# Kernel tuning notes

Measured on AMD Instinct MI355X. Metric: run time of the kernel, lower is better.

Reference implementation:

```python
import jax, jax.numpy as jnp
import numpy as np

B = 64          # graphs in batch
NVARS = 256     # variables per graph
LITS_PER = 2 * NVARS
NL = B * LITS_PER      # 32768 literals
CLS_PER = 1024
NC = B * CLS_PER       # 65536 clauses
K = 3                  # literals per clause (3-CNF)
D = 128
NUM_ITERS = 8


def setup_inputs() -> dict:
    key = jax.random.key(0)
    ks = jax.random.split(key, 16)
    # edge list of the sparse clause-literal incidence matrix adj_t [NC, NL]
    edge_clause = jnp.repeat(jnp.arange(NC, dtype=jnp.int32), K)            # [E]
    clause_graph = jnp.repeat(jnp.arange(NC, dtype=jnp.int32) // CLS_PER, K)
    lit_local = jax.random.randint(ks[0], (NC * K,), 0, LITS_PER, dtype=jnp.int32)
    edge_lit = clause_graph * LITS_PER + lit_local                          # [E]
    s = 0.05
    inp = {
        "edge_clause": edge_clause,
        "edge_lit": edge_lit,
        "x_l0": jax.random.uniform(ks[1], (NL, D), jnp.float32),
        "x_c0": jax.random.uniform(ks[2], (NC, D), jnp.float32),
        "W_ih_lc": jax.random.normal(ks[3], (D, D), jnp.float32) * s,
        "W_hh_lc": jax.random.normal(ks[4], (D, D), jnp.float32) * s,
        "b_ih_lc": jax.random.normal(ks[5], (D,), jnp.float32) * s,
        "b_hh_lc": jax.random.normal(ks[6], (D,), jnp.float32) * s,
        "W_ih_cl": jax.random.normal(ks[7], (D, 2 * D), jnp.float32) * s,
        "W_hh_cl": jax.random.normal(ks[8], (D, D), jnp.float32) * s,
        "b_ih_cl": jax.random.normal(ks[9], (D,), jnp.float32) * s,
        "b_hh_cl": jax.random.normal(ks[10], (D,), jnp.float32) * s,
        "L_vote_w": jax.random.normal(ks[11], (1, D), jnp.float32) * s,
        "L_vote_b": jax.random.normal(ks[12], (1,), jnp.float32) * s,
        "true_vec_w": jax.random.normal(ks[13], (1, D), jnp.float32) * s,
        "num_iters": NUM_ITERS,
    }
    return inp


def _l2norm(x):
    return x / jnp.linalg.norm(x, axis=1, keepdims=True)


def _rnn_cell(x, h, Wih, Whh, bih, bhh):
    # torch nn.RNN (tanh) single step: h' = tanh(x W_ih^T + b_ih + h W_hh^T + b_hh)
    return jnp.tanh(x @ Wih.T + bih + h @ Whh.T + bhh)


def _flip(x_l):
    # per graph, swap [pos vars | neg vars] halves
    return x_l.reshape(B, 2, NVARS, D)[:, ::-1].reshape(NL, D)


def reference(edge_clause, edge_lit, x_l0, x_c0,
              W_ih_lc, W_hh_lc, b_ih_lc, b_hh_lc,
              W_ih_cl, W_hh_cl, b_ih_cl, b_hh_cl,
              L_vote_w, L_vote_b, true_vec_w, num_iters):
    x_l = _l2norm(x_l0)
    x_c = _l2norm(x_c0)

    truth0 = x_l @ true_vec_w.T          # [NL, 1]
    clause0 = x_c                        # [NC, D]

    def step(carry, _):
        x_l, x_c = carry
        # LC: clause messages = adj_t @ x_l  (sparse matmul as gather+segment_sum)
        msg_c = jax.ops.segment_sum(x_l[edge_lit], edge_clause, num_segments=NC)
        x_c_new = _rnn_cell(msg_c, x_c, W_ih_lc, W_hh_lc, b_ih_lc, b_hh_lc)
        # CL: literal messages = adj_t^T @ x_c_new
        msg_l = jax.ops.segment_sum(x_c_new[edge_clause], edge_lit, num_segments=NL)
        inp = jnp.concatenate([msg_l, _flip(x_l)], axis=1)   # [NL, 2D]
        x_l_new = _rnn_cell(inp, x_l, W_ih_cl, W_hh_cl, b_ih_cl, b_hh_cl)
        x_l_n = _l2norm(x_l_new)
        x_c_n = _l2norm(x_c_new)
        truth = x_l_n @ true_vec_w.T                          # [NL, 1]
        return (x_l_n, x_c_n), (truth, x_c_n)

    (x_l, x_c), (truths, clauses) = jax.lax.scan(step, (x_l, x_c), None, length=num_iters)

    truth_all = jnp.concatenate([truth0[None], truths], axis=0)    # [T+1, NL, 1]
    clause_all = jnp.concatenate([clause0[None], clauses], axis=0)  # [T+1, NC, D]

    x_l_vote = x_l @ L_vote_w.T + L_vote_b                   # [NL, 1]
    vote_mean_pool = x_l_vote.reshape(B, LITS_PER, 1).mean(axis=1)  # [B, 1]

    # ragged per-graph lists in the original are contiguous blocks here;
    # we return the flat concatenations (identical data).
    return (x_l_vote, x_l, vote_mean_pool, truth_all[-1], truth_all, clause_all, truth_all[0])
```

## Files before the change

### kernel.cpp

```cpp
#include <hip/hip_runtime.h>
#include <math.h>

namespace {
constexpr int NVARS    = 256;
constexpr int LITS_PER = 2 * NVARS;
constexpr int Bg       = 64;
constexpr int NL       = Bg * LITS_PER;
constexpr int CLS_PER  = 1024;
constexpr int NC       = Bg * CLS_PER;
constexpr int NE       = NC * 3;
constexpr int D        = 128;
constexpr int T        = 8;

constexpr size_t OFF_VOTE  = 0;
constexpr size_t OFF_XL    = (size_t)NL;
constexpr size_t OFF_POOL  = OFF_XL + (size_t)NL * D;
constexpr size_t OFF_TLAST = OFF_POOL + Bg;
constexpr size_t OFF_TALL  = OFF_TLAST + NL;
constexpr size_t OFF_CALL  = OFF_TALL + (size_t)(T + 1) * NL;
constexpr size_t OFF_T0    = OFF_CALL + (size_t)(T + 1) * NC * D;

constexpr int PKM    = 16384;
constexpr int PK_TOT = 5 * PKM;
constexpr size_t SHM_LC = 2 * PKM * sizeof(unsigned short);
constexpr size_t SHM_CL = 2 * PKM * sizeof(unsigned short) + 1536;
}

typedef __attribute__((ext_vector_type(8))) short short8v;
typedef __attribute__((ext_vector_type(4))) float f32x4;

__device__ __forceinline__ unsigned short f2bf(float v) {
    unsigned u = __float_as_uint(v);
    return (unsigned short)((u + 0x7fffu + ((u >> 16) & 1u)) >> 16);
}
__device__ __forceinline__ float bf2f(unsigned short b) {
    return __uint_as_float(((unsigned)b) << 16);
}
__device__ __forceinline__ void cvt_frag(const float (&v)[8], short8v& ah, short8v& al) {
    #pragma unroll
    for (int j = 0; j < 8; j++) {
        unsigned short h = f2bf(v[j]);
        ah[j] = (short)h;
        al[j] = (short)f2bf(v[j] - bf2f(h));
    }
}
__device__ __forceinline__ float ftanh(float x) {
    float e = __builtin_amdgcn_exp2f(x * 2.885390081777926814f);
    return 1.0f - 2.0f * __builtin_amdgcn_rcpf(e + 1.0f);
}
__device__ __forceinline__ void mm2(f32x4& c, short8v ah, short8v al,
                                    const unsigned short* buf, int off) {
    short8v b = *(const short8v*)(buf + off);
    c = __builtin_amdgcn_mfma_f32_16x16x32_bf16(ah, b, c, 0, 0, 0);
    c = __builtin_amdgcn_mfma_f32_16x16x32_bf16(al, b, c, 0, 0, 0);
}

__global__ __launch_bounds__(256) void pack5(
    const float* __restrict__ ihlc, const float* __restrict__ hhlc,
    const float* __restrict__ hhcl, const float* __restrict__ ihcl,
    unsigned short* __restrict__ pk) {
    int idx = blockIdx.x * 256 + threadIdx.x;
    int mat = idx >> 14, rel = idx & 16383;
    int j = rel & 7, lane = (rel >> 3) & 63, ks = (rel >> 9) & 3, n = rel >> 11;
    int r = n * 16 + (lane & 15);
    int k = ks * 32 + (lane >> 4) * 8 + j;
    float w;
    if (mat == 0)      w = ihlc[r * 128 + k];
    else if (mat == 1) w = hhlc[r * 128 + k];
    else if (mat == 2) w = hhcl[r * 128 + k];
    else if (mat == 3) w = ihcl[r * 256 + k];
    else               w = ihcl[r * 256 + 128 + k];
    pk[mat * PKM + rel] = f2bf(w);
}

__global__ void csr_count(const int* __restrict__ edge_lit, int* __restrict__ counts) {
    int e = blockIdx.x * blockDim.x + threadIdx.x;
    if (e < NE) atomicAdd(&counts[edge_lit[e]], 1);
}

__global__ __launch_bounds__(1024) void csr_scan(const int* __restrict__ counts,
                                                 int* __restrict__ offs,
                                                 int* __restrict__ cursor) {
    __shared__ int part[1024];
    const int t = threadIdx.x;
    const int base = t * 32;
    int local[32];
    int s = 0;
    for (int i = 0; i < 32; i++) { local[i] = s; s += counts[base + i]; }
    part[t] = s;
    __syncthreads();
    for (int d = 1; d < 1024; d <<= 1) {
        int v = 0;
        if (t >= d) v = part[t - d];
        __syncthreads();
        if (t >= d) part[t] += v;
        __syncthreads();
    }
    const int excl = (t == 0) ? 0 : part[t - 1];
    for (int i = 0; i < 32; i++) {
        int o = excl + local[i];
        offs[base + i] = o;
        cursor[base + i] = o;
    }
    if (t == 1023) offs[NL] = part[1023];
}

__global__ void csr_fill(const int* __restrict__ edge_lit, int* __restrict__ cursor,
                         int* __restrict__ csr) {
    int e = blockIdx.x * blockDim.x + threadIdx.x;
    if (e < NE) {
        int l = edge_lit[e];
        int p = atomicAdd(&cursor[l], 1);
        csr[p] = e / 3;
    }
}

__global__ void csr_sort(const int* __restrict__ offs, int* __restrict__ csr) {
    int l = blockIdx.x * blockDim.x + threadIdx.x;
    if (l >= NL) return;
    int s = offs[l], e = offs[l + 1];
    for (int i = s + 1; i < e; i++) {
        int v = csr[i];
        int j = i - 1;
        while (j >= s && csr[j] > v) { csr[j + 1] = csr[j]; j--; }
        csr[j + 1] = v;
    }
}

__global__ __launch_bounds__(64) void make_perm(const int* __restrict__ counts,
                                                int* __restrict__ perm) {
    __shared__ int d[64];
    const int b = blockIdx.x, i = threadIdx.x;
    d[i] = counts[b * 64 + i];
    __syncthreads();
    const int di = d[i];
    int rank = 0;
    for (int j = 0; j < 64; j++) {
        int dj = d[j];
        rank += (dj < di) || (dj == di && j < i);
    }
    perm[b * 64 + rank] = i;
}

__global__ void rownorm_dot(const float* __restrict__ in, float* __restrict__ out,
                            unsigned short* __restrict__ out_bf,
                            const float* __restrict__ dotw, float* __restrict__ dot0,
                            float* __restrict__ dot1, int nrows) {
    int wave = (int)((blockIdx.x * blockDim.x + threadIdx.x) >> 6);
    int lane = threadIdx.x & 63;
    if (wave >= nrows) return;
    const float* r = in + (size_t)wave * D;
    float v0 = r[lane], v1 = r[lane + 64];
    float ss = v0 * v0 + v1 * v1;
    #pragma unroll
    for (int m = 32; m; m >>= 1) ss += __shfl_xor(ss, m);
    float rn = 1.0f / sqrtf(ss);
    float y0 = v0 * rn, y1 = v1 * rn;
    float* o = out + (size_t)wave * D;
    o[lane] = y0;
    o[lane + 64] = y1;
    if (out_bf) {
        unsigned short* ob = out_bf + (size_t)wave * D;
        ob[lane] = f2bf(y0);
        ob[lane + 64] = f2bf(y1);
    }
    if (dotw) {
        float dv = y0 * dotw[lane] + y1 * dotw[lane + 64];
        #pragma unroll
        for (int m = 32; m; m >>= 1) dv += __shfl_xor(dv, m);
        if (lane == 0) {
            dot0[wave] = dv;
            if (dot1) dot1[wave] = dv;
        }
    }
}

__device__ __forceinline__ void gather3b(const int* __restrict__ ep,
                                         const unsigned short* __restrict__ xlb,
                                         int arow, int g, float (&v)[4][8]) {
    int e0 = ep[3 * arow], e1 = ep[3 * arow + 1], e2 = ep[3 * arow + 2];
    const unsigned short* r0 = xlb + (size_t)e0 * D + g * 8;
    const unsigned short* r1 = xlb + (size_t)e1 * D + g * 8;
    const unsigned short* r2 = xlb + (size_t)e2 * D + g * 8;
    #pragma unroll
    for (int ks = 0; ks < 4; ks++) {
        short8v a = *(const short8v*)(r0 + ks * 32);
        short8v b = *(const short8v*)(r1 + ks * 32);
        short8v c = *(const short8v*)(r2 + ks * 32);
        #pragma unroll
        for (int j = 0; j < 8; j++)
            v[ks][j] = bf2f((unsigned short)a[j]) + bf2f((unsigned short)b[j]) +
                       bf2f((unsigned short)c[j]);
    }
}

__device__ __forceinline__ void loadrow(const float* __restrict__ rp, float (&v)[4][8]) {
    #pragma unroll
    for (int ks = 0; ks < 4; ks++) {
        float4 a = *(const float4*)(rp + ks * 32), b = *(const float4*)(rp + ks * 32 + 4);
        v[ks][0] = a.x; v[ks][1] = a.y; v[ks][2] = a.z; v[ks][3] = a.w;
        v[ks][4] = b.x; v[ks][5] = b.y; v[ks][6] = b.z; v[ks][7] = b.w;
    }
}

__device__ __forceinline__ void gatherCSRb(const int* __restrict__ offs,
                                           const int* __restrict__ csr,
                                           const unsigned short* __restrict__ xcb,
                                           int arow, int g, float (&v)[4][8]) {
    #pragma unroll
    for (int ks = 0; ks < 4; ks++)
        #pragma unroll
        for (int j = 0; j < 8; j++) v[ks][j] = 0.f;
    const int s = offs[arow], e = offs[arow + 1];
    for (int p = s; p < e; p++) {
        const unsigned short* q = xcb + (size_t)csr[p] * D + g * 8;
        #pragma unroll
        for (int ks = 0; ks < 4; ks++) {
            short8v a = *(const short8v*)(q + ks * 32);
            #pragma unroll
            for (int j = 0; j < 8; j++) v[ks][j] += bf2f((unsigned short)a[j]);
        }
    }
}

__global__ __launch_bounds__(512, 4) void lc_mfma(
    const int* __restrict__ edge_lit, const unsigned short* __restrict__ xl_bf,
    const float* __restrict__ xc_prev, const unsigned short* __restrict__ pk,
    const float* __restrict__ bih, const float* __restrict__ bhh,
    float* __restrict__ xc_norm, unsigned short* __restrict__ xc_bf) {
    extern __shared__ __align__(16) unsigned short lds[];
    const int tid = threadIdx.x, wid = tid >> 6, lane = tid & 63;
    const int m = lane & 15, g = lane >> 4;
    const int p = blockIdx.x;
    const int blk = (p & 7) * 64 + (p >> 3);
    const int rowbase = blk * 128;
    const int arow = rowbase + wid * 16 + m;

    {
        const short8v* src = (const short8v*)pk;
        short8v* dst = (short8v*)lds;
        #pragma unroll
        for (int i = 0; i < 8; i++) dst[i * 512 + tid] = src[i * 512 + tid];
    }
    float v[4][8];
    gather3b(edge_lit, xl_bf, arow, g, v);
    float vh[4][8];
    loadrow(xc_prev + (size_t)arow * D + g * 8, vh);
    __syncthreads();

    short8v ah[4], al[4];
    #pragma unroll
    for (int ks = 0; ks < 4; ks++) cvt_frag(v[ks], ah[ks], al[ks]);

    f32x4 acc[8];
    #pragma unroll
    for (int n = 0; n < 8; n++) acc[n] = (f32x4)0.f;

    #pragma unroll
    for (int ks = 0; ks < 4; ks++)
        #pragma unroll
        for (int n = 0; n < 8; n++)
            mm2(acc[n], ah[ks], al[ks], lds, ((n * 4 + ks) * 64 + lane) * 8);

    #pragma unroll
    for (int ks = 0; ks < 4; ks++) cvt_frag(vh[ks], ah[ks], al[ks]);
    #pragma unroll
    for (int ks = 0; ks < 4; ks++)
        #pragma unroll
        for (int n = 0; n < 8; n++)
            mm2(acc[n], ah[ks], al[ks], lds + PKM, ((n * 4 + ks) * 64 + lane) * 8);

    float bias[8];
    #pragma unroll
    for (int n = 0; n < 8; n++) bias[n] = bih[n * 16 + m] + bhh[n * 16 + m];

    const int obase = rowbase + wid * 16 + g * 4;
    #pragma unroll
    for (int r = 0; r < 4; r++) {
        float w[8], ss = 0.f;
        #pragma unroll
        for (int n = 0; n < 8; n++) { w[n] = ftanh(acc[n][r] + bias[n]); ss += w[n] * w[n]; }
        ss += __shfl_xor(ss, 1); ss += __shfl_xor(ss, 2);
        ss += __shfl_xor(ss, 4); ss += __shfl_xor(ss, 8);
        const float rn = __builtin_amdgcn_rsqf(ss);
        const size_t rowoff = (size_t)(obase + r) * D + m;
        #pragma unroll
        for (int n = 0; n < 8; n++) {
            xc_norm[rowoff + n * 16] = w[n] * rn;
            xc_bf[rowoff + n * 16] = f2bf(w[n]);
        }
    }
}

__global__ __launch_bounds__(512, 4) void cl_mfma(
    const int* __restrict__ offs, const int* __restrict__ csr,
    const int* __restrict__ perm,
    const unsigned short* __restrict__ xc_bf,
    const float* __restrict__ xl, const unsigned short* __restrict__ pk,
    const float* __restrict__ bih, const float* __restrict__ bhh,
    const float* __restrict__ tv, const float* __restrict__ vw,
    const float* __restrict__ vb,
    float* __restrict__ xl_out, unsigned short* __restrict__ xl_bf,
    float* __restrict__ truth, float* __restrict__ truth2, float* __restrict__ vote) {
    extern __shared__ __align__(16) unsigned short lds[];
    float* scr = (float*)(lds + 2 * PKM);
    float* ssx = scr; float* twx = scr + 128; float* vwx = scr + 256;

    const int tid = threadIdx.x, wid = tid >> 6, lane = tid & 63;
    const int m = lane & 15, g = lane >> 4;
    const int rw = wid >> 1, nh = wid & 1, nbase = nh * 4;
    const int p0 = blockIdx.x;
    const int blk = (p0 & 7) * 64 + (p0 >> 3);
    const int lbase = blk * 64;
    const int arow = lbase + perm[lbase + rw * 16 + m];

    {
        const short8v* srcA = (const short8v*)(pk + 3 * PKM);
        const short8v* srcB = (const short8v*)(pk + 2 * PKM);
        short8v* d0 = (short8v*)lds;
        short8v* d1 = (short8v*)(lds + PKM);
        #pragma unroll
        for (int i = 0; i < 4; i++) d0[i * 512 + tid] = srcA[i * 512 + tid];
        #pragma unroll
        for (int i = 0; i < 4; i++) d1[i * 512 + tid] = srcB[i * 512 + tid];
    }
    float v[4][8];
    gatherCSRb(offs, csr, xc_bf, arow, g, v);
    __syncthreads();

    short8v ah[4], al[4];
    #pragma unroll
    for (int ks = 0; ks < 4; ks++) cvt_frag(v[ks], ah[ks], al[ks]);

    f32x4 acc[4];
    #pragma unroll
    for (int n = 0; n < 4; n++) acc[n] = (f32x4)0.f;

    short8v fr[4];
    {
        const short8v* srcF = (const short8v*)(pk + 4 * PKM);
        #pragma unroll
        for (int i = 0; i < 4; i++) fr[i] = srcF[i * 512 + tid];
    }
    float vh[4][8];
    loadrow(xl + (size_t)arow * D + g * 8, vh);

    #pragma unroll
    for (int ks = 0; ks < 4; ks++)
        #pragma unroll
        for (int nn = 0; nn < 4; nn++)
            mm2(acc[nn], ah[ks], al[ks], lds, (((nbase + nn) * 4 + ks) * 64 + lane) * 8);

    __syncthreads();
    {
        short8v* d0 = (short8v*)lds;
        #pragma unroll
        for (int i = 0; i < 4; i++) d0[i * 512 + tid] = fr[i];
    }
    #pragma unroll
    for (int ks = 0; ks < 4; ks++) cvt_frag(vh[ks], ah[ks], al[ks]);

    float vf[4][8];
    loadrow(xl + (size_t)(arow ^ 256) * D + g * 8, vf);

    #pragma unroll
    for (int ks = 0; ks < 4; ks++)
        #pragma unroll
        for (int nn = 0; nn < 4; nn++)
            mm2(acc[nn], ah[ks], al[ks], lds + PKM, (((nbase + nn) * 4 + ks) * 64 + lane) * 8);

    __syncthreads();
    #pragma unroll
    for (int ks = 0; ks < 4; ks++) cvt_frag(vf[ks], ah[ks], al[ks]);
    #pragma unroll
    for (int ks = 0; ks < 4; ks++)
        #pragma unroll
        for (int nn = 0; nn < 4; nn++)
            mm2(acc[nn], ah[ks], al[ks], lds, (((nbase + nn) * 4 + ks) * 64 + lane) * 8);

    float bias[4], tvv[4], vwv[4];
    #pragma unroll
    for (int nn = 0; nn < 4; nn++) {
        int n = nbase + nn;
        bias[nn] = bih[n * 16 + m] + bhh[n * 16 + m];
        tvv[nn] = tv[n * 16 + m];
        vwv[nn] = vote ? vw[n * 16 + m] : 0.f;
    }
    float wv[4][4];
    #pragma unroll
    for (int r = 0; r < 4; r++) {
        float ssp = 0.f, twp = 0.f, vwp = 0.f;
        #pragma unroll
        for (int nn = 0; nn < 4; nn++) {
            float w = ftanh(acc[nn][r] + bias[nn]);
            wv[r][nn] = w;
            ssp += w * w; twp += w * tvv[nn]; vwp += w * vwv[nn];
        }
        ssp += __shfl_xor(ssp, 1); ssp += __shfl_xor(ssp, 2);
        ssp += __shfl_xor(ssp, 4); ssp += __shfl_xor(ssp, 8);
        twp += __shfl_xor(twp, 1); twp += __shfl_xor(twp, 2);
        twp += __shfl_xor(twp, 4); twp += __shfl_xor(twp, 8);
        if (vote) {
            vwp += __shfl_xor(vwp, 1); vwp += __shfl_xor(vwp, 2);
            vwp += __shfl_xor(vwp, 4); vwp += __shfl_xor(vwp, 8);
        }
        if (m == 0) {
            int rl = rw * 16 + g * 4 + r;
            ssx[rl * 2 + nh] = ssp;
            twx[rl * 2 + nh] = twp;
            if (vote) vwx[rl * 2 + nh] = vwp;
        }
    }
    __syncthreads();
    const float vb0 = vote ? vb[0] : 0.f;
    #pragma unroll
    for (int r = 0; r < 4; r++) {
        const int rl = rw * 16 + g * 4 + r;
        const int grow = lbase + perm[lbase + rl];
        const float ss = ssx[rl * 2] + ssx[rl * 2 + 1];
        const float rn = __builtin_amdgcn_rsqf(ss);
        const size_t rowoff = (size_t)grow * D + m;
        #pragma unroll
        for (int nn = 0; nn < 4; nn++) {
            const float y = wv[r][nn] * rn;
            xl_out[rowoff + (nbase + nn) * 16] = y;
            xl_bf[rowoff + (nbase + nn) * 16] = f2bf(y);
        }
        if (m == 0 && nh == 0) {
            const float td = rn * (twx[rl * 2] + twx[rl * 2 + 1]);
            truth[grow] = td;
            if (truth2) truth2[grow] = td;
            if (vote) vote[grow] = rn * (vwx[rl * 2] + vwx[rl * 2 + 1]) + vb0;
        }
    }
}

__global__ void pool_kernel(const float* __restrict__ votes, float* __restrict__ pool) {
    __shared__ float s[4];
    int g = blockIdx.x, t = threadIdx.x;
    float v = votes[g * LITS_PER + t] + votes[g * LITS_PER + 256 + t];
    #pragma unroll
    for (int m = 32; m; m >>= 1) v += __shfl_xor(v, m);
    if ((t & 63) == 0) s[t >> 6] = v;
    __syncthreads();
    if (t == 0) pool[g] = (s[0] + s[1] + s[2] + s[3]) * (1.0f / LITS_PER);
}

extern "C" void kernel_launch(void* const* d_in, const int* in_sizes, int n_in,
                              void* d_out, int out_size, void* d_ws, size_t ws_size,
                              hipStream_t stream) {
    const int*   edge_lit = (const int*)d_in[1];
    const float* x_l0     = (const float*)d_in[2];
    const float* x_c0     = (const float*)d_in[3];
    const float* W_ih_lc  = (const float*)d_in[4];
    const float* W_hh_lc  = (const float*)d_in[5];
    const float* b_ih_lc  = (const float*)d_in[6];
    const float* b_hh_lc  = (const float*)d_in[7];
    const float* W_ih_cl  = (const float*)d_in[8];
    const float* W_hh_cl  = (const float*)d_in[9];
    const float* b_ih_cl  = (const float*)d_in[10];
    const float* b_hh_cl  = (const float*)d_in[11];
    const float* L_vote_w = (const float*)d_in[12];
    const float* L_vote_b = (const float*)d_in[13];
    const float* true_vec = (const float*)d_in[14];

    float* out   = (float*)d_out;
    float* xl_o  = out + OFF_XL;
    float* call  = out + OFF_CALL;
    float* tall  = out + OFF_TALL;

    float* xl_ws = (float*)d_ws;
    unsigned short* xc_bf = (unsigned short*)(xl_ws + (size_t)NL * D);
    unsigned short* xl_bf = xc_bf + (size_t)NC * D;
    unsigned short* pk = xl_bf + (size_t)NL * D;
    int* counts = (int*)(pk + PK_TOT);
    int* offs   = counts + NL;
    int* cursor = offs + NL + 1;
    int* csr    = cursor + NL;
    int* perm   = csr + NE;

    hipMemsetAsync(counts, 0, NL * sizeof(int), stream);

    pack5<<<PK_TOT / 256, 256, 0, stream>>>(W_ih_lc, W_hh_lc, W_hh_cl, W_ih_cl, pk);
    csr_count<<<NE / 256, 256, 0, stream>>>(edge_lit, counts);
    csr_scan<<<1, 1024, 0, stream>>>(counts, offs, cursor);
    csr_fill<<<NE / 256, 256, 0, stream>>>(edge_lit, cursor, csr);
    csr_sort<<<NL / 256, 256, 0, stream>>>(offs, csr);
    make_perm<<<NL / 64, 64, 0, stream>>>(counts, perm);

    rownorm_dot<<<NL / 4, 256, 0, stream>>>(x_l0, xl_o, xl_bf, true_vec, tall,
                                            out + OFF_T0, NL);
    rownorm_dot<<<NC / 4, 256, 0, stream>>>(x_c0, call, nullptr, nullptr, nullptr,
                                            nullptr, NC);

    for (int t = 1; t <= T; t++) {
        const float* xl_src = (t & 1) ? xl_o : xl_ws;
        float*       xl_dst = (t & 1) ? xl_ws : xl_o;
        lc_mfma<<<NC / 128, 512, SHM_LC, stream>>>(
            edge_lit, xl_bf, call + (size_t)(t - 1) * NC * D, pk,
            b_ih_lc, b_hh_lc, call + (size_t)t * NC * D, xc_bf);
        cl_mfma<<<NL / 64, 512, SHM_CL, stream>>>(
            offs, csr, perm, xc_bf, xl_src, pk,
            b_ih_cl, b_hh_cl, true_vec, L_vote_w, L_vote_b,
            xl_dst, xl_bf, tall + (size_t)t * NL,
            (t == T) ? out + OFF_TLAST : nullptr,
            (t == T) ? out + OFF_VOTE : nullptr);
    }

    pool_kernel<<<Bg, 256, 0, stream>>>(out + OFF_VOTE, out + OFF_POOL);
}
```

Before: 564.4 us.

## Feed recurrent hidden states as bf16 with cached norms instead of fp32 reloads

The literal-to-clause kernel now reads the previous clause state from the bf16 unnormalized buffer and rescales it by a stored per-row norm, instead of reloading the fp32 normalized output. The clause-to-literal kernel reads its own hidden state and the flipped state as bf16 from ping-pong buffers and uses single bf16 MFMAs instead of hi/lo split pairs. The fp32 literal state is written only on the final iteration. This cuts fp32 global reads, intermediate writes and half the MFMAs on the hidden-state paths, at the cost of bf16 rounding on recurrent inputs, which may reduce accuracy.

Result: faster. 510.0 us (-9.6%).

```diff
diff --git a/kernel.cpp b/kernel.cpp
--- a/kernel.cpp
+++ b/kernel.cpp
@@ -53,6 +53,11 @@
     short8v b = *(const short8v*)(buf + off);
     c = __builtin_amdgcn_mfma_f32_16x16x32_bf16(ah, b, c, 0, 0, 0);
     c = __builtin_amdgcn_mfma_f32_16x16x32_bf16(al, b, c, 0, 0, 0);
+}
+__device__ __forceinline__ void mm1(f32x4& c, short8v a,
+                                    const unsigned short* buf, int off) {
+    short8v b = *(const short8v*)(buf + off);
+    c = __builtin_amdgcn_mfma_f32_16x16x32_bf16(a, b, c, 0, 0, 0);
 }
 
 __global__ __launch_bounds__(256) void pack5(
@@ -144,6 +149,7 @@
 
 __global__ void rownorm_dot(const float* __restrict__ in, float* __restrict__ out,
                             unsigned short* __restrict__ out_bf,
+                            float* __restrict__ norms,
                             const float* __restrict__ dotw, float* __restrict__ dot0,
                             float* __restrict__ dot1, int nrows) {
     int wave = (int)((blockIdx.x * blockDim.x + threadIdx.x) >> 6);
@@ -159,8 +165,12 @@
     float* o = out + (size_t)wave * D;
     o[lane] = y0;
     o[lane + 64] = y1;
-    if (out_bf) {
-        unsigned short* ob = out_bf + (size_t)wave * D;
+    unsigned short* ob = out_bf + (size_t)wave * D;
+    if (norms) {
+        ob[lane] = f2bf(v0);
+        ob[lane + 64] = f2bf(v1);
+        if (lane == 0) norms[wave] = ss * rn;
+    } else {
         ob[lane] = f2bf(y0);
         ob[lane + 64] = f2bf(y1);
     }
@@ -194,15 +204,6 @@
     }
 }
 
-__device__ __forceinline__ void loadrow(const float* __restrict__ rp, float (&v)[4][8]) {
-    #pragma unroll
-    for (int ks = 0; ks < 4; ks++) {
-        float4 a = *(const float4*)(rp + ks * 32), b = *(const float4*)(rp + ks * 32 + 4);
-        v[ks][0] = a.x; v[ks][1] = a.y; v[ks][2] = a.z; v[ks][3] = a.w;
-        v[ks][4] = b.x; v[ks][5] = b.y; v[ks][6] = b.z; v[ks][7] = b.w;
-    }
-}
-
 __device__ __forceinline__ void gatherCSRb(const int* __restrict__ offs,
                                            const int* __restrict__ csr,
                                            const unsigned short* __restrict__ xcb,
@@ -225,9 +226,10 @@
 
 __global__ __launch_bounds__(512, 4) void lc_mfma(
     const int* __restrict__ edge_lit, const unsigned short* __restrict__ xl_bf,
-    const float* __restrict__ xc_prev, const unsigned short* __restrict__ pk,
+    unsigned short* xc_bf, float* norms,
+    const unsigned short* __restrict__ pk,
     const float* __restrict__ bih, const float* __restrict__ bhh,
-    float* __restrict__ xc_norm, unsigned short* __restrict__ xc_bf) {
+    float* __restrict__ xc_norm) {
     extern __shared__ __align__(16) unsigned short lds[];
     const int tid = threadIdx.x, wid = tid >> 6, lane = tid & 63;
     const int m = lane & 15, g = lane >> 4;
@@ -244,8 +246,13 @@
     }
     float v[4][8];
     gather3b(edge_lit, xl_bf, arow, g, v);
-    float vh[4][8];
-    loadrow(xc_prev + (size_t)arow * D + g * 8, vh);
+    short8v hvb[4];
+    {
+        const unsigned short* hr = xc_bf + (size_t)arow * D + g * 8;
+        #pragma unroll
+        for (int ks = 0; ks < 4; ks++) hvb[ks] = *(const short8v*)(hr + ks * 32);
+    }
+    const float rnh = __builtin_amdgcn_rcpf(norms[arow]);
     __syncthreads();
 
     short8v ah[4], al[4];
@@ -262,6 +269,12 @@
         for (int n = 0; n < 8; n++)
             mm2(acc[n], ah[ks], al[ks], lds, ((n * 4 + ks) * 64 + lane) * 8);
 
+    float vh[4][8];
+    #pragma unroll
+    for (int ks = 0; ks < 4; ks++)
+        #pragma unroll
+        for (int j = 0; j < 8; j++)
+            vh[ks][j] = bf2f((unsigned short)hvb[ks][j]) * rnh;
     #pragma unroll
     for (int ks = 0; ks < 4; ks++) cvt_frag(vh[ks], ah[ks], al[ks]);
     #pragma unroll
@@ -289,6 +302,7 @@
             xc_norm[rowoff + n * 16] = w[n] * rn;
             xc_bf[rowoff + n * 16] = f2bf(w[n]);
         }
+        if (m == 0) norms[obase + r] = ss * rn;
     }
 }
 
@@ -296,11 +310,13 @@
     const int* __restrict__ offs, const int* __restrict__ csr,
     const int* __restrict__ perm,
     const unsigned short* __restrict__ xc_bf,
-    const float* __restrict__ xl, const unsigned short* __restrict__ pk,
+    const unsigned short* __restrict__ xl_src,
+    const unsigned short* __restrict__ pk,
     const float* __restrict__ bih, const float* __restrict__ bhh,
     const float* __restrict__ tv, const float* __restrict__ vw,
     const float* __restrict__ vb,
-    float* __restrict__ xl_out, unsigned short* __restrict__ xl_bf,
+    unsigned short* __restrict__ xl_dst,
+    float* __restrict__ xl_out,
     float* __restrict__ truth, float* __restrict__ truth2, float* __restrict__ vote) {
     extern __shared__ __align__(16) unsigned short lds[];
     float* scr = (float*)(lds + 2 * PKM);
@@ -326,6 +342,14 @@
     }
     float v[4][8];
     gatherCSRb(offs, csr, xc_bf, arow, g, v);
+    short8v hv[4], fv[4];
+    {
+        const unsigned short* hr = xl_src + (size_t)arow * D + g * 8;
+        const unsigned short* fp = xl_src + (size_t)(arow ^ 256) * D + g * 8;
+        #pragma unroll
+        for (int ks = 0; ks < 4; ks++) { hv[ks] = *(const short8v*)(hr + ks * 32);
+                                         fv[ks] = *(const short8v*)(fp + ks * 32); }
+    }
     __syncthreads();
 
     short8v ah[4], al[4];
@@ -342,8 +366,6 @@
         #pragma unroll
         for (int i = 0; i < 4; i++) fr[i] = srcF[i * 512 + tid];
     }
-    float vh[4][8];
-    loadrow(xl + (size_t)arow * D + g * 8, vh);
 
     #pragma unroll
     for (int ks = 0; ks < 4; ks++)
@@ -358,25 +380,17 @@
         for (int i = 0; i < 4; i++) d0[i * 512 + tid] = fr[i];
     }
     #pragma unroll
-    for (int ks = 0; ks < 4; ks++) cvt_frag(vh[ks], ah[ks], al[ks]);
-
-    float vf[4][8];
-    loadrow(xl + (size_t)(arow ^ 256) * D + g * 8, vf);
-
-    #pragma unroll
     for (int ks = 0; ks < 4; ks++)
         #pragma unroll
         for (int nn = 0; nn < 4; nn++)
-            mm2(acc[nn], ah[ks], al[ks], lds + PKM, (((nbase + nn) * 4 + ks) * 64 + lane) * 8);
-
-    __syncthreads();
-    #pragma unroll
-    for (int ks = 0; ks < 4; ks++) cvt_frag(vf[ks], ah[ks], al[ks]);
+            mm1(acc[nn], hv[ks], lds + PKM, (((nbase + nn) * 4 + ks) * 64 + lane) * 8);
+
+    __syncthreads();
     #pragma unroll
     for (int ks = 0; ks < 4; ks++)
         #pragma unroll
         for (int nn = 0; nn < 4; nn++)
-            mm2(acc[nn], ah[ks], al[ks], lds, (((nbase + nn) * 4 + ks) * 64 + lane) * 8);
+            mm1(acc[nn], fv[ks], lds, (((nbase + nn) * 4 + ks) * 64 + lane) * 8);
 
     float bias[4], tvv[4], vwv[4];
     #pragma unroll
@@ -423,8 +437,8 @@
         #pragma unroll
         for (int nn = 0; nn < 4; nn++) {
             const float y = wv[r][nn] * rn;
-            xl_out[rowoff + (nbase + nn) * 16] = y;
-            xl_bf[rowoff + (nbase + nn) * 16] = f2bf(y);
+            xl_dst[rowoff + (nbase + nn) * 16] = f2bf(y);
+            if (xl_out) xl_out[rowoff + (nbase + nn) * 16] = y;
         }
         if (m == 0 && nh == 0) {
             const float td = rn * (twx[rl * 2] + twx[rl * 2 + 1]);
@@ -469,11 +483,12 @@
     float* call  = out + OFF_CALL;
     float* tall  = out + OFF_TALL;
 
-    float* xl_ws = (float*)d_ws;
-    unsigned short* xc_bf = (unsigned short*)(xl_ws + (size_t)NL * D);
-    unsigned short* xl_bf = xc_bf + (size_t)NC * D;
-    unsigned short* pk = xl_bf + (size_t)NL * D;
-    int* counts = (int*)(pk + PK_TOT);
+    unsigned short* xc_bf  = (unsigned short*)d_ws;
+    unsigned short* xl_bf0 = xc_bf + (size_t)NC * D;
+    unsigned short* xl_bf1 = xl_bf0 + (size_t)NL * D;
+    unsigned short* pk     = xl_bf1 + (size_t)NL * D;
+    float* norms = (float*)(pk + PK_TOT);
+    int* counts = (int*)(norms + NC);
     int* offs   = counts + NL;
     int* cursor = offs + NL + 1;
     int* csr    = cursor + NL;
@@ -488,21 +503,21 @@
     csr_sort<<<NL / 256, 256, 0, stream>>>(offs, csr);
     make_perm<<<NL / 64, 64, 0, stream>>>(counts, perm);
 
-    rownorm_dot<<<NL / 4, 256, 0, stream>>>(x_l0, xl_o, xl_bf, true_vec, tall,
-                                            out + OFF_T0, NL);
-    rownorm_dot<<<NC / 4, 256, 0, stream>>>(x_c0, call, nullptr, nullptr, nullptr,
-                                            nullptr, NC);
+    rownorm_dot<<<NL / 4, 256, 0, stream>>>(x_l0, xl_o, xl_bf0, nullptr, true_vec,
+                                            tall, out + OFF_T0, NL);
+    rownorm_dot<<<NC / 4, 256, 0, stream>>>(x_c0, call, xc_bf, norms, nullptr,
+                                            nullptr, nullptr, NC);
 
     for (int t = 1; t <= T; t++) {
-        const float* xl_src = (t & 1) ? xl_o : xl_ws;
-        float*       xl_dst = (t & 1) ? xl_ws : xl_o;
+        const unsigned short* src = (t & 1) ? xl_bf0 : xl_bf1;
+        unsigned short*       dst = (t & 1) ? xl_bf1 : xl_bf0;
         lc_mfma<<<NC / 128, 512, SHM_LC, stream>>>(
-            edge_lit, xl_bf, call + (size_t)(t - 1) * NC * D, pk,
-            b_ih_lc, b_hh_lc, call + (size_t)t * NC * D, xc_bf);
+            edge_lit, src, xc_bf, norms, pk, b_ih_lc, b_hh_lc,
+            call + (size_t)t * NC * D);
         cl_mfma<<<NL / 64, 512, SHM_CL, stream>>>(
-            offs, csr, perm, xc_bf, xl_src, pk,
+            offs, csr, perm, xc_bf, src, pk,
             b_ih_cl, b_hh_cl, true_vec, L_vote_w, L_vote_b,
-            xl_dst, xl_bf, tall + (size_t)t * NL,
+            dst, (t == T) ? xl_o : nullptr, tall + (size_t)t * NL,
             (t == T) ? out + OFF_TLAST : nullptr,
             (t == T) ? out + OFF_VOTE : nullptr);
     }
```
